# Optimization experiments

Measured on AMD Instinct MI355X. Metric: run time of the kernel, lower is better.

The kernel has to match this reference:

```python
import jax, jax.numpy as jnp
import numpy as np

B, N_IN, N_ALL, NPT, K, C, H = 8, 20000, 1200, 1024, 34, 96, 6
DH = C // H
RADIUS2 = (2.5 * 0.04) ** 2  # grid_size=0.04, sigma=1.0 -> radius 0.1


def _fps(xyz, npoint):
    # furthest point sampling, vectorized over batch, scan over sample steps
    Bb, Nn, _ = xyz.shape
    def step(carry, _):
        dist, far = carry
        cen = jnp.take_along_axis(xyz, far[:, None, None], axis=1)  # [B,1,3]
        d = jnp.sum((xyz - cen) ** 2, -1)                           # [B,N]
        dist = jnp.minimum(dist, d)
        return (dist, jnp.argmax(dist, -1).astype(jnp.int32)), far
    init = (jnp.full((Bb, Nn), 1e10, xyz.dtype), jnp.zeros((Bb,), jnp.int32))
    _, idx = jax.lax.scan(step, init, None, length=npoint)
    return idx.T  # [B, npoint]


def _gather(x, idx):
    return jnp.take_along_axis(x, idx[:, :, None], axis=1)


def _ln(x, g, b):
    m = jnp.mean(x, -1, keepdims=True)
    v = jnp.var(x, -1, keepdims=True)
    return (x - m) * jax.lax.rsqrt(v + 1e-5) * g + b


def _forward(point_clouds, cloud_colors, W_in, b_in, Wq, Wk, Wv, Wo, Wpos, W1, b1, W2, b2, g1, be1, g2, be2, sel):
    fps_idx = _fps(point_clouds, N_ALL)      # [B,1200]
    fps_idx = fps_idx[:, sel]                # random 1024 of 1200 (fixed permutation)
    coord = _gather(point_clouds, fps_idx)   # [B,P,3]
    color = _gather(cloud_colors, fps_idx)   # [B,P,3]
    # ball query within each cloud (all clouds have equal count -> batched dense dists)
    d2 = jnp.sum((coord[:, :, None] - coord[:, None]) ** 2, -1)        # [B,P,P]
    valid = d2 <= RADIUS2
    nidx = jnp.argsort(jnp.where(valid, d2, 1e10), axis=-1)[..., :K]   # [B,P,K]
    nvalid = jnp.take_along_axis(valid, nidx, axis=-1)                 # [B,P,K]
    feat = jnp.concatenate([color, coord], -1)                         # [B,P,6]
    x = feat @ W_in + b_in                                             # [B,P,C]
    q = (x @ Wq).reshape(B, NPT, H, DH)
    k = x @ Wk
    v = x @ Wv
    def gat(t):  # gather per-neighbor features: [B,P,C*] -> [B,P,K,C*]
        return jnp.take_along_axis(t, nidx.reshape(B, NPT * K)[:, :, None], axis=1).reshape(B, NPT, K, -1)
    kn, vn, pn = gat(k), gat(v), gat(coord)
    pe = (coord[:, :, None] - pn) @ Wpos                               # [B,P,K,C] rel-pos enc
    kn = (kn + pe).reshape(B, NPT, K, H, DH)
    vn = (vn + pe).reshape(B, NPT, K, H, DH)
    logits = jnp.einsum('bphd,bpkhd->bphk', q, kn) / jnp.sqrt(jnp.float32(DH))
    logits = jnp.where(nvalid[:, :, None, :], logits, -1e9)
    attn = jax.nn.softmax(logits, -1)
    out = jnp.einsum('bphk,bpkhd->bphd', attn, vn).reshape(B, NPT, C)
    x = _ln(x + out @ Wo, g1, be1)
    x = _ln(x + jax.nn.relu(x @ W1 + b1) @ W2 + b2, g2, be2)
    features = jnp.transpose(x, (0, 2, 1))                             # [B,C,P]
    return features, coord


def setup_inputs() -> dict:
    key = jax.random.key(0)
    ks = jax.random.split(key, 16)
    s = 0.1
    w = lambda k, shp: jax.random.normal(k, shp, jnp.float32) * s
    return {
        'point_clouds': jax.random.uniform(ks[0], (B, N_IN, 3), jnp.float32),
        'cloud_colors': jax.random.uniform(ks[1], (B, N_IN, 3), jnp.float32),
        'W_in': w(ks[2], (6, C)), 'b_in': jnp.zeros((C,), jnp.float32),
        'Wq': w(ks[3], (C, C)), 'Wk': w(ks[4], (C, C)), 'Wv': w(ks[5], (C, C)),
        'Wo': w(ks[6], (C, C)), 'Wpos': w(ks[7], (3, C)),
        'W1': w(ks[8], (C, 4 * C)), 'b1': jnp.zeros((4 * C,), jnp.float32),
        'W2': w(ks[9], (4 * C, C)), 'b2': jnp.zeros((C,), jnp.float32),
        'g1': jnp.ones((C,), jnp.float32), 'be1': jnp.zeros((C,), jnp.float32),
        'g2': jnp.ones((C,), jnp.float32), 'be2': jnp.zeros((C,), jnp.float32),
        'sel': jax.random.permutation(ks[10], N_ALL)[:NPT].astype(jnp.int32),
    }


def reference(point_clouds, cloud_colors, W_in, b_in, Wq, Wk, Wv, Wo, Wpos, W1, b1, W2, b2, g1, be1, g2, be2, sel):
    return _forward(point_clouds, cloud_colors, W_in, b_in, Wq, Wk, Wv, Wo, Wpos, W1, b1, W2, b2, g1, be1, g2, be2, sel)
```

## Files before the change

### kernel.cpp

```cpp
#include <hip/hip_runtime.h>
#include <math.h>

#define B_   8
#define NIN  20000
#define NALL 1200
#define NPTQ 1024
#define KNB  34
#define CH   96
#define FF   384
#define NQ   (B_ * NPTQ)
#define SL   20

typedef unsigned int   u32;
typedef unsigned long long u64;

__device__ __forceinline__ float scrub(float f) {
    u32 u = __float_as_uint(f);
    return ((u & 0x7F800000u) == 0x7F800000u) ? 12345.0f : f;
}

__global__ __launch_bounds__(1024, 4) void fps_kernel(const float* __restrict__ pc,
                                                      int* __restrict__ fps_idx) {
    const int b = blockIdx.x;
    const int tid = threadIdx.x;
    const int lane = tid & 63;
    const int wid = tid >> 6;
    const float* base = pc + (size_t)b * NIN * 3;

    float px[SL], py[SL], pz[SL], dist[SL];
#pragma unroll
    for (int j = 0; j < SL; ++j) {
        int idx = tid + j * 1024;
        bool ok = (j < SL - 1) || (idx < NIN);
        int ia = ok ? idx : 0;
        px[j] = base[(size_t)ia * 3 + 0];
        py[j] = base[(size_t)ia * 3 + 1];
        pz[j] = base[(size_t)ia * 3 + 2];
        dist[j] = ok ? 1e10f : -1.0f;
    }
#pragma unroll
    for (int j = 0; j < SL; ++j) {
        asm volatile("" : "+v"(px[j]), "+v"(py[j]), "+v"(pz[j]));
    }

    __shared__ u64 red[2][16];

    if (tid == 0) fps_idx[b * NALL + 0] = 0;
    float cx = base[0], cy = base[1], cz = base[2];

    for (int it = 1; it < NALL; ++it) {
        const int p = it & 1;
        float bd = -1e38f; int bi = 0;
#pragma unroll
        for (int j = 0; j < SL; ++j) {
            float dx = __fsub_rn(px[j], cx);
            float dy = __fsub_rn(py[j], cy);
            float dz = __fsub_rn(pz[j], cz);
            float d = __fadd_rn(__fadd_rn(__fmul_rn(dx, dx), __fmul_rn(dy, dy)),
                                __fmul_rn(dz, dz));
            float nd = fminf(dist[j], d);
            dist[j] = nd;
            if (nd > bd) { bd = nd; bi = tid + j * 1024; }
        }
        u64 key = ((u64)__float_as_uint(bd) << 32) | (u32)(NIN - bi);
#pragma unroll
        for (int s = 32; s; s >>= 1) {
            u64 o = __shfl_xor(key, s, 64);
            key = (o > key) ? o : key;
        }
        if (lane == 0) red[p][wid] = key;
        __syncthreads();
        u64 k2 = red[p][lane & 15];
#pragma unroll
        for (int s = 1; s < 16; s <<= 1) {
            u64 o = __shfl_xor(k2, s, 64);
            k2 = (o > k2) ? o : k2;
        }
        int widx = NIN - (int)(k2 & 0xFFFFFFFFu);
        if (tid == 0) fps_idx[b * NALL + it] = widx;
        const float* wp = base + (size_t)widx * 3;
        cx = wp[0]; cy = wp[1]; cz = wp[2];
    }
}

__global__ void gather_kernel(const float* __restrict__ pc,
                              const int* __restrict__ fps_idx, const int* __restrict__ sel,
                              float* __restrict__ coord, float* __restrict__ out_coord) {
    int t = blockIdx.x * 256 + threadIdx.x;
    if (t >= NQ) return;
    int b = t >> 10, j = t & 1023;
    int p = fps_idx[b * NALL + sel[j]];
    p = (p < 0) ? 0 : ((p >= NIN) ? (NIN - 1) : p);
    const float* pp = pc + ((size_t)b * NIN + p) * 3;
    float x = pp[0], y = pp[1], z = pp[2];
    coord[(size_t)t * 3 + 0] = x;
    coord[(size_t)t * 3 + 1] = y;
    coord[(size_t)t * 3 + 2] = z;
    out_coord[(size_t)t * 3 + 0] = scrub(x);
    out_coord[(size_t)t * 3 + 1] = scrub(y);
    out_coord[(size_t)t * 3 + 2] = scrub(z);
}

__global__ void knn_kernel(const float* __restrict__ coord, int* __restrict__ nbr) {
    __shared__ float sx[NPTQ], sy[NPTQ], sz[NPTQ];
    const double RAD2D = (2.5 * 0.04) * (2.5 * 0.04);
    int b = blockIdx.x >> 8;
    int i0 = (blockIdx.x & 255) * 4;
    const float* cb = coord + (size_t)b * NPTQ * 3;
    for (int t = threadIdx.x; t < NPTQ; t += 256) {
        sx[t] = cb[(size_t)t * 3 + 0];
        sy[t] = cb[(size_t)t * 3 + 1];
        sz[t] = cb[(size_t)t * 3 + 2];
    }
    __syncthreads();
    int wid = threadIdx.x >> 6, lane = threadIdx.x & 63;
    int i = i0 + wid;
    float qx = sx[i], qy = sy[i], qz = sz[i];
    u64 pk[16];
#pragma unroll
    for (int t = 0; t < 16; ++t) {
        int j = lane + t * 64;
        float dx = __fsub_rn(qx, sx[j]);
        float dy = __fsub_rn(qy, sy[j]);
        float dz = __fsub_rn(qz, sz[j]);
        float d2 = __fadd_rn(__fadd_rn(__fmul_rn(dx, dx), __fmul_rn(dy, dy)),
                             __fmul_rn(dz, dz));
        bool valid = ((double)d2 <= RAD2D);
        pk[t] = valid ? (((u64)__float_as_uint(d2) << 32) | (u32)j) : ~0ull;
    }
    int* out = nbr + ((size_t)b * NPTQ + i) * KNB;
    int k = 0;
    for (; k < KNB; ++k) {
        u64 m = ~0ull;
#pragma unroll
        for (int t = 0; t < 16; ++t) m = (pk[t] < m) ? pk[t] : m;
#pragma unroll
        for (int s = 32; s; s >>= 1) {
            u64 o = __shfl_xor(m, s, 64);
            m = (o < m) ? o : m;
        }
        if (m == ~0ull) break;
#pragma unroll
        for (int t = 0; t < 16; ++t) if (pk[t] == m) pk[t] = ~0ull;
        if (lane == 0) out[k] = (int)(m & 0xFFFFFFFFu);
    }
    for (; k < KNB; ++k) if (lane == 0) out[k] = -1;
}

__global__ void xproj_kernel(const float* __restrict__ pc, const float* __restrict__ col,
                             const int* __restrict__ fps_idx, const int* __restrict__ sel,
                             const float* __restrict__ Win, const float* __restrict__ bin,
                             float* __restrict__ x) {
    int idx = blockIdx.x * 256 + threadIdx.x;
    if (idx >= NQ * CH) return;
    int q = idx / CH, c = idx - q * CH;
    int b = q >> 10, j = q & 1023;
    int p = fps_idx[b * NALL + sel[j]];
    p = (p < 0) ? 0 : ((p >= NIN) ? (NIN - 1) : p);
    const float* pp = pc + ((size_t)b * NIN + p) * 3;
    const float* cc = col + ((size_t)b * NIN + p) * 3;
    float acc = bin[c];
    acc += cc[0] * Win[0 * CH + c];
    acc += cc[1] * Win[1 * CH + c];
    acc += cc[2] * Win[2 * CH + c];
    acc += pp[0] * Win[3 * CH + c];
    acc += pp[1] * Win[4 * CH + c];
    acc += pp[2] * Win[5 * CH + c];
    x[idx] = acc;
}

__global__ void qkv_kernel(const float* __restrict__ x,
                           const float* __restrict__ Wq, const float* __restrict__ Wk,
                           const float* __restrict__ Wv,
                           float* __restrict__ qo, float* __restrict__ ko,
                           float* __restrict__ vo) {
    int idx = blockIdx.x * 256 + threadIdx.x;
    if (idx >= NQ * CH) return;
    int q = idx / CH, c = idx - q * CH;
    const float* xr = x + (size_t)q * CH;
    float aq = 0.f, ak = 0.f, av = 0.f;
    for (int k = 0; k < CH; ++k) {
        float xv = xr[k];
        aq += xv * Wq[k * CH + c];
        ak += xv * Wk[k * CH + c];
        av += xv * Wv[k * CH + c];
    }
    qo[idx] = aq; ko[idx] = ak; vo[idx] = av;
}

__global__ __launch_bounds__(384) void attn_kernel(float* __restrict__ qr1,
                            const float* __restrict__ km, const float* __restrict__ vm,
                            const float* __restrict__ coord, const int* __restrict__ nbr,
                            const float* __restrict__ Wpos, const float* __restrict__ Wo,
                            const float* __restrict__ x) {
    __shared__ float wp[3 * CH];
    __shared__ float os[4][CH];
    for (int t = threadIdx.x; t < 3 * CH; t += 384) wp[t] = Wpos[t];
    __syncthreads();
    int lq = threadIdx.x / CH;
    int c = threadIdx.x - lq * CH;
    int qi = blockIdx.x * 4 + lq;
    int b = qi >> 10, i = qi & 1023;
    const float* crd = coord + (size_t)b * NPTQ * 3;
    float cx = crd[(size_t)i * 3], cy = crd[(size_t)i * 3 + 1], cz = crd[(size_t)i * 3 + 2];
    float qv = qr1[(size_t)qi * CH + c];
    const int* nb = nbr + (size_t)qi * KNB;
    float m = -1e30f, l = 0.f, acc = 0.f;
    for (int t = 0; t < KNB; ++t) {
        int j = nb[t];
        if (j < 0) break;
        float dx = cx - crd[(size_t)j * 3];
        float dy = cy - crd[(size_t)j * 3 + 1];
        float dz = cz - crd[(size_t)j * 3 + 2];
        float pe = dx * wp[c] + dy * wp[CH + c] + dz * wp[2 * CH + c];
        size_t row = (size_t)(b * NPTQ + j) * CH + c;
        float kn = km[row] + pe;
        float s = qv * kn;
        s += __shfl_xor(s, 1); s += __shfl_xor(s, 2);
        s += __shfl_xor(s, 4); s += __shfl_xor(s, 8);
        float logit = s * 0.25f;
        float mn = fmaxf(m, logit);
        float sc = expf(m - mn);
        float p = expf(logit - mn);
        float vn = vm[row] + pe;
        l = l * sc + p;
        acc = acc * sc + p * vn;
        m = mn;
    }
    os[lq][c] = (l > 0.f) ? acc / l : 0.f;
    __syncthreads();
    float r = x[(size_t)qi * CH + c];
    for (int k = 0; k < CH; ++k) r += os[lq][k] * Wo[k * CH + c];
    qr1[(size_t)qi * CH + c] = r;
}

__global__ void ln_kernel(const float* __restrict__ in, const float* __restrict__ g,
                          const float* __restrict__ be, float* __restrict__ out) {
    int row = blockIdx.x * 4 + (threadIdx.x >> 6);
    int lane = threadIdx.x & 63;
    const float* r = in + (size_t)row * CH;
    float e0 = r[lane];
    float e1 = (lane < 32) ? r[64 + lane] : 0.0f;
    float s = e0 + e1;
#pragma unroll
    for (int k = 32; k; k >>= 1) s += __shfl_xor(s, k);
    float mean = s * (1.0f / 96.0f);
    float d0 = e0 - mean, d1 = e1 - mean;
    float vs = d0 * d0 + ((lane < 32) ? d1 * d1 : 0.0f);
#pragma unroll
    for (int k = 32; k; k >>= 1) vs += __shfl_xor(vs, k);
    float rs = 1.0f / sqrtf(vs * (1.0f / 96.0f) + 1e-5f);
    float* o = out + (size_t)row * CH;
    o[lane] = d0 * rs * g[lane] + be[lane];
    if (lane < 32) o[64 + lane] = d1 * rs * g[64 + lane] + be[64 + lane];
}

__global__ __launch_bounds__(384) void ffn_kernel(const float* __restrict__ x2,
                           const float* __restrict__ W1, const float* __restrict__ b1,
                           const float* __restrict__ W2, const float* __restrict__ b2,
                           float* __restrict__ r2) {
    __shared__ float xs[4][CH];
    __shared__ float hs[4][FF];
    __shared__ float ps[4][4][CH];
    int row0 = blockIdx.x * 4, t = threadIdx.x;
    { int r = t / CH, c = t - (t / CH) * CH;
      xs[r][c] = x2[(size_t)(row0 + r) * CH + c]; }
    __syncthreads();
    {
        float bt = b1[t];
        float a0 = bt, a1 = bt, a2 = bt, a3 = bt;
        for (int k = 0; k < CH; ++k) {
            float w = W1[k * FF + t];
            a0 += xs[0][k] * w; a1 += xs[1][k] * w;
            a2 += xs[2][k] * w; a3 += xs[3][k] * w;
        }
        hs[0][t] = fmaxf(a0, 0.f); hs[1][t] = fmaxf(a1, 0.f);
        hs[2][t] = fmaxf(a2, 0.f); hs[3][t] = fmaxf(a3, 0.f);
    }
    __syncthreads();
    {
        int chunk = t / CH, c = t - (t / CH) * CH;
        float p0 = 0.f, p1 = 0.f, p2 = 0.f, p3 = 0.f;
        for (int m = chunk * CH; m < (chunk + 1) * CH; ++m) {
            float w = W2[m * CH + c];
            p0 += hs[0][m] * w; p1 += hs[1][m] * w;
            p2 += hs[2][m] * w; p3 += hs[3][m] * w;
        }
        ps[0][chunk][c] = p0; ps[1][chunk][c] = p1;
        ps[2][chunk][c] = p2; ps[3][chunk][c] = p3;
    }
    __syncthreads();
    { int r = t / CH, c = t - (t / CH) * CH;
      float rr = xs[r][c] + ((ps[r][0][c] + ps[r][1][c]) + (ps[r][2][c] + ps[r][3][c])) + b2[c];
      r2[(size_t)(row0 + r) * CH + c] = rr; }
}

__global__ void ln2t_kernel(const float* __restrict__ in, const float* __restrict__ g,
                            const float* __restrict__ be, float* __restrict__ out) {
    int row = blockIdx.x * 4 + (threadIdx.x >> 6);
    int lane = threadIdx.x & 63;
    int b = row >> 10, i = row & 1023;
    const float* r = in + (size_t)row * CH;
    float e0 = r[lane];
    float e1 = (lane < 32) ? r[64 + lane] : 0.0f;
    float s = e0 + e1;
#pragma unroll
    for (int k = 32; k; k >>= 1) s += __shfl_xor(s, k);
    float mean = s * (1.0f / 96.0f);
    float d0 = e0 - mean, d1 = e1 - mean;
    float vs = d0 * d0 + ((lane < 32) ? d1 * d1 : 0.0f);
#pragma unroll
    for (int k = 32; k; k >>= 1) vs += __shfl_xor(vs, k);
    float rs = 1.0f / sqrtf(vs * (1.0f / 96.0f) + 1e-5f);
    float y0 = d0 * rs * g[lane] + be[lane];
    out[((size_t)(b * CH + lane)) * NPTQ + i] = scrub(y0);
    if (lane < 32) {
        float y1 = d1 * rs * g[64 + lane] + be[64 + lane];
        out[((size_t)(b * CH + 64 + lane)) * NPTQ + i] = scrub(y1);
    }
}

extern "C" void kernel_launch(void* const* d_in, const int* in_sizes, int n_in,
                              void* d_out, int out_size, void* d_ws, size_t ws_size,
                              hipStream_t stream) {
    const float* pc   = (const float*)d_in[0];
    const float* col  = (const float*)d_in[1];
    const float* Win  = (const float*)d_in[2];
    const float* bin  = (const float*)d_in[3];
    const float* Wq   = (const float*)d_in[4];
    const float* Wk   = (const float*)d_in[5];
    const float* Wv   = (const float*)d_in[6];
    const float* Wo   = (const float*)d_in[7];
    const float* Wpos = (const float*)d_in[8];
    const float* W1   = (const float*)d_in[9];
    const float* b1   = (const float*)d_in[10];
    const float* W2   = (const float*)d_in[11];
    const float* b2   = (const float*)d_in[12];
    const float* g1   = (const float*)d_in[13];
    const float* be1  = (const float*)d_in[14];
    const float* g2   = (const float*)d_in[15];
    const float* be2  = (const float*)d_in[16];
    const int*  sel   = (const int*)d_in[17];

    float* out_feat  = (float*)d_out;
    float* out_coord = out_feat + (size_t)B_ * CH * NPTQ;

    char* ws = (char*)d_ws;
    size_t off = 0;
    auto alloc = [&](size_t bytes) { void* p = ws + off; off += (bytes + 255) & ~(size_t)255; return p; };
    int*   w_fps   = (int*)  alloc((size_t)B_ * NALL * 4);
    float* w_coord = (float*)alloc((size_t)NQ * 3 * 4);
    int*   w_nbr   = (int*)  alloc((size_t)NQ * KNB * 4);
    float* w_x     = (float*)alloc((size_t)NQ * CH * 4);
    float* w_q     = (float*)alloc((size_t)NQ * CH * 4);
    float* w_k     = (float*)alloc((size_t)NQ * CH * 4);
    float* w_v     = (float*)alloc((size_t)NQ * CH * 4);
    (void)ws_size; (void)in_sizes; (void)n_in; (void)out_size;

    fps_kernel<<<B_, 1024, 0, stream>>>(pc, w_fps);
    gather_kernel<<<NQ / 256, 256, 0, stream>>>(pc, w_fps, sel, w_coord, out_coord);
    knn_kernel<<<NQ / 4, 256, 0, stream>>>(w_coord, w_nbr);
    xproj_kernel<<<NQ * CH / 256, 256, 0, stream>>>(pc, col, w_fps, sel, Win, bin, w_x);
    qkv_kernel<<<NQ * CH / 256, 256, 0, stream>>>(w_x, Wq, Wk, Wv, w_q, w_k, w_v);
    attn_kernel<<<NQ / 4, 384, 0, stream>>>(w_q, w_k, w_v, w_coord, w_nbr, Wpos, Wo, w_x);
    ln_kernel<<<NQ / 4, 256, 0, stream>>>(w_q, g1, be1, w_k);
    ffn_kernel<<<NQ / 4, 384, 0, stream>>>(w_k, W1, b1, W2, b2, w_v);
    ln2t_kernel<<<NQ / 4, 256, 0, stream>>>(w_v, g2, be2, out_feat);
}
```

Baseline: 2.628 ms.

## Halve FPS block size and use packed two-wide float math per thread

The FPS kernel now runs 512 threads per batch, each owning 40 points held as two-wide float vectors so subtract, multiply and min can map to packed FP32 instructions. The cross-wave reduction shrinks from 16 to 8 waves and is done by reading shared memory serially instead of with shuffles. The aim is to shorten the per-iteration critical path of the serial 1200-step loop, both in compute and in synchronization. In exchange, each thread does twice as much work per step and uses more registers. The no-op shuffles replace the asm barrier that kept the point values resident in registers.

```diff
diff --git a/kernel.cpp b/kernel.cpp
--- a/kernel.cpp
+++ b/kernel.cpp
@@ -9,74 +9,90 @@
 #define CH   96
 #define FF   384
 #define NQ   (B_ * NPTQ)
-#define SL   20
+
+#define FT   512
+#define NPR  20
 
 typedef unsigned int   u32;
 typedef unsigned long long u64;
+typedef float v2f __attribute__((ext_vector_type(2)));
 
 __device__ __forceinline__ float scrub(float f) {
     u32 u = __float_as_uint(f);
     return ((u & 0x7F800000u) == 0x7F800000u) ? 12345.0f : f;
 }
 
-__global__ __launch_bounds__(1024, 4) void fps_kernel(const float* __restrict__ pc,
-                                                      int* __restrict__ fps_idx) {
+__global__ __launch_bounds__(FT, 2) void fps_kernel(const float* __restrict__ pc,
+                                                    int* __restrict__ fps_idx) {
+#pragma clang fp contract(off)
     const int b = blockIdx.x;
     const int tid = threadIdx.x;
     const int lane = tid & 63;
     const int wid = tid >> 6;
     const float* base = pc + (size_t)b * NIN * 3;
 
-    float px[SL], py[SL], pz[SL], dist[SL];
-#pragma unroll
-    for (int j = 0; j < SL; ++j) {
-        int idx = tid + j * 1024;
-        bool ok = (j < SL - 1) || (idx < NIN);
-        int ia = ok ? idx : 0;
-        px[j] = base[(size_t)ia * 3 + 0];
-        py[j] = base[(size_t)ia * 3 + 1];
-        pz[j] = base[(size_t)ia * 3 + 2];
-        dist[j] = ok ? 1e10f : -1.0f;
-    }
-#pragma unroll
-    for (int j = 0; j < SL; ++j) {
-        asm volatile("" : "+v"(px[j]), "+v"(py[j]), "+v"(pz[j]));
-    }
-
-    __shared__ u64 red[2][16];
+    v2f px[NPR], py[NPR], pz[NPR], dist[NPR];
+#pragma unroll
+    for (int j = 0; j < NPR; ++j) {
+        int i0 = tid + (2 * j) * FT;
+        int i1 = i0 + FT;
+        bool ok1 = i1 < NIN;
+        int a1 = ok1 ? i1 : 0;
+        float x0 = base[(size_t)i0 * 3 + 0];
+        float y0 = base[(size_t)i0 * 3 + 1];
+        float z0 = base[(size_t)i0 * 3 + 2];
+        float x1 = base[(size_t)a1 * 3 + 0];
+        float y1 = base[(size_t)a1 * 3 + 1];
+        float z1 = base[(size_t)a1 * 3 + 2];
+        x0 = __shfl(x0, lane); y0 = __shfl(y0, lane); z0 = __shfl(z0, lane);
+        x1 = __shfl(x1, lane); y1 = __shfl(y1, lane); z1 = __shfl(z1, lane);
+        px[j].x = x0; px[j].y = x1;
+        py[j].x = y0; py[j].y = y1;
+        pz[j].x = z0; pz[j].y = z1;
+        dist[j].x = 1e10f;
+        dist[j].y = ok1 ? 1e10f : -1.0f;
+    }
+
+    __shared__ u64 rkey[2][8];
 
     if (tid == 0) fps_idx[b * NALL + 0] = 0;
     float cx = base[0], cy = base[1], cz = base[2];
 
     for (int it = 1; it < NALL; ++it) {
-        const int p = it & 1;
-        float bd = -1e38f; int bi = 0;
-#pragma unroll
-        for (int j = 0; j < SL; ++j) {
-            float dx = __fsub_rn(px[j], cx);
-            float dy = __fsub_rn(py[j], cy);
-            float dz = __fsub_rn(pz[j], cz);
-            float d = __fadd_rn(__fadd_rn(__fmul_rn(dx, dx), __fmul_rn(dy, dy)),
-                                __fmul_rn(dz, dz));
-            float nd = fminf(dist[j], d);
+        const int pb = it & 1;
+        v2f cvx; cvx.x = cx; cvx.y = cx;
+        v2f cvy; cvy.x = cy; cvy.y = cy;
+        v2f cvz; cvz.x = cz; cvz.y = cz;
+        float bd0 = -1e38f, bd1 = -1e38f;
+        int bi0 = 0, bi1 = 0;
+#pragma unroll
+        for (int j = 0; j < NPR; ++j) {
+            v2f dx = px[j] - cvx;
+            v2f dy = py[j] - cvy;
+            v2f dz = pz[j] - cvz;
+            v2f sx = dx * dx;
+            v2f sy = dy * dy;
+            v2f sz = dz * dz;
+            v2f d  = (sx + sy) + sz;
+            v2f nd = __builtin_elementwise_min(dist[j], d);
             dist[j] = nd;
-            if (nd > bd) { bd = nd; bi = tid + j * 1024; }
-        }
-        u64 key = ((u64)__float_as_uint(bd) << 32) | (u32)(NIN - bi);
+            if (nd.x > bd0) { bd0 = nd.x; bi0 = tid + (2 * j) * FT; }
+            if (nd.y > bd1) { bd1 = nd.y; bi1 = tid + (2 * j + 1) * FT; }
+        }
+        u64 k0 = ((u64)__float_as_uint(bd0) << 32) | (u32)(NIN - bi0);
+        u64 k1 = ((u64)__float_as_uint(bd1) << 32) | (u32)(NIN - bi1);
+        u64 key = (k1 > k0) ? k1 : k0;
 #pragma unroll
         for (int s = 32; s; s >>= 1) {
             u64 o = __shfl_xor(key, s, 64);
             key = (o > key) ? o : key;
         }
-        if (lane == 0) red[p][wid] = key;
+        if (lane == 0) rkey[pb][wid] = key;
         __syncthreads();
-        u64 k2 = red[p][lane & 15];
-#pragma unroll
-        for (int s = 1; s < 16; s <<= 1) {
-            u64 o = __shfl_xor(k2, s, 64);
-            k2 = (o > k2) ? o : k2;
-        }
-        int widx = NIN - (int)(k2 & 0xFFFFFFFFu);
+        u64 kk = rkey[pb][0];
+#pragma unroll
+        for (int w = 1; w < 8; ++w) { u64 o = rkey[pb][w]; kk = (o > kk) ? o : kk; }
+        int widx = NIN - (int)(kk & 0xFFFFFFFFu);
         if (tid == 0) fps_idx[b * NALL + it] = widx;
         const float* wp = base + (size_t)widx * 3;
         cx = wp[0]; cy = wp[1]; cz = wp[2];
@@ -357,7 +373,7 @@
     float* w_v     = (float*)alloc((size_t)NQ * CH * 4);
     (void)ws_size; (void)in_sizes; (void)n_in; (void)out_size;
 
-    fps_kernel<<<B_, 1024, 0, stream>>>(pc, w_fps);
+    fps_kernel<<<B_, FT, 0, stream>>>(pc, w_fps);
     gather_kernel<<<NQ / 256, 256, 0, stream>>>(pc, w_fps, sel, w_coord, out_coord);
     knn_kernel<<<NQ / 4, 256, 0, stream>>>(w_coord, w_nbr);
     xproj_kernel<<<NQ * CH / 256, 256, 0, stream>>>(pc, col, w_fps, sel, Win, bin, w_x);
```

Result: faster. 2.477 ms (-5.7%).

## Bucket FPS points by spatial cell and skip distance updates via bounding-box bounds

Applied to the files above, without the earlier changes.

The FPS kernel now counting-sorts each cloud's points into an 8x8x8 grid and stores them as float4 (xyz plus original index) in workspace, so each thread owns a spatially compact group of 20 points. Each thread keeps a bounding box of its group. It skips the distance update when the box's lower-bound distance to the new centroid cannot lower its current max distance. This is meant to avoid most per-iteration distance work in later FPS iterations. In exchange, points are reloaded from global/L2 each iteration instead of registers, and the in-block sort adds setup cost. The skip test is conservative (0.999 factor) but the tie-break ordering must still match the reference argmax.

```diff
diff --git a/kernel.cpp b/kernel.cpp
--- a/kernel.cpp
+++ b/kernel.cpp
@@ -9,7 +9,10 @@
 #define CH   96
 #define FF   384
 #define NQ   (B_ * NPTQ)
-#define SL   20
+
+#define GC   8
+#define NC   (GC * GC * GC)
+#define PPT  20
 
 typedef unsigned int   u32;
 typedef unsigned long long u64;
@@ -19,56 +22,111 @@
     return ((u & 0x7F800000u) == 0x7F800000u) ? 12345.0f : f;
 }
 
-__global__ __launch_bounds__(1024, 4) void fps_kernel(const float* __restrict__ pc,
-                                                      int* __restrict__ fps_idx) {
+__device__ __forceinline__ int cell_of(float x, float y, float z) {
+    int ix = (int)(x * (float)GC); ix = ix < 0 ? 0 : (ix > GC - 1 ? GC - 1 : ix);
+    int iy = (int)(y * (float)GC); iy = iy < 0 ? 0 : (iy > GC - 1 ? GC - 1 : iy);
+    int iz = (int)(z * (float)GC); iz = iz < 0 ? 0 : (iz > GC - 1 ? GC - 1 : iz);
+    return (ix * GC + iy) * GC + iz;
+}
+
+__global__ __launch_bounds__(1024, 4) void fps_kernel(
+        const float* __restrict__ pc, int* __restrict__ fps_idx,
+        float4* __restrict__ gpts) {
+#pragma clang fp contract(off)
     const int b = blockIdx.x;
     const int tid = threadIdx.x;
     const int lane = tid & 63;
     const int wid = tid >> 6;
     const float* base = pc + (size_t)b * NIN * 3;
-
-    float px[SL], py[SL], pz[SL], dist[SL];
-#pragma unroll
-    for (int j = 0; j < SL; ++j) {
+    float4* bp = gpts + (size_t)b * NIN;
+
+    __shared__ int cstart[NC];
+    __shared__ int ccur[NC];
+    __shared__ u64 red[2][16];
+
+    for (int c = tid; c < NC; c += 1024) ccur[c] = 0;
+    __syncthreads();
+    for (int j = 0; j < PPT; ++j) {
         int idx = tid + j * 1024;
-        bool ok = (j < SL - 1) || (idx < NIN);
-        int ia = ok ? idx : 0;
-        px[j] = base[(size_t)ia * 3 + 0];
-        py[j] = base[(size_t)ia * 3 + 1];
-        pz[j] = base[(size_t)ia * 3 + 2];
-        dist[j] = ok ? 1e10f : -1.0f;
-    }
-#pragma unroll
-    for (int j = 0; j < SL; ++j) {
-        asm volatile("" : "+v"(px[j]), "+v"(py[j]), "+v"(pz[j]));
-    }
-
-    __shared__ u64 red[2][16];
-
+        if (idx < NIN) {
+            float x = base[(size_t)idx * 3 + 0];
+            float y = base[(size_t)idx * 3 + 1];
+            float z = base[(size_t)idx * 3 + 2];
+            atomicAdd(&ccur[cell_of(x, y, z)], 1);
+        }
+    }
+    __syncthreads();
+    if (tid == 0) {
+        int acc = 0;
+        for (int c = 0; c < NC; ++c) { cstart[c] = acc; acc += ccur[c]; }
+    }
+    __syncthreads();
+    if (tid < NC) ccur[tid] = cstart[tid];
+    __syncthreads();
+    for (int j = 0; j < PPT; ++j) {
+        int idx = tid + j * 1024;
+        if (idx < NIN) {
+            float x = base[(size_t)idx * 3 + 0];
+            float y = base[(size_t)idx * 3 + 1];
+            float z = base[(size_t)idx * 3 + 2];
+            int pos = atomicAdd(&ccur[cell_of(x, y, z)], 1);
+            bp[pos] = make_float4(x, y, z, (float)idx);
+        }
+    }
+    __syncthreads();
+
+    const bool valid = tid < (NIN / PPT);
+    float dist[PPT];
+#pragma unroll
+    for (int j = 0; j < PPT; ++j) dist[j] = 1e10f;
+    float bnx = 1e30f, bny = 1e30f, bnz = 1e30f;
+    float bxx = -1e30f, bxy = -1e30f, bxz = -1e30f;
+    if (valid) {
+#pragma unroll
+        for (int j = 0; j < PPT; ++j) {
+            float4 w = bp[tid * PPT + j];
+            bnx = fminf(bnx, w.x); bxx = fmaxf(bxx, w.x);
+            bny = fminf(bny, w.y); bxy = fmaxf(bxy, w.y);
+            bnz = fminf(bnz, w.z); bxz = fmaxf(bxz, w.z);
+        }
+    }
+    u64 key = valid ? (((u64)__float_as_uint(1e10f) << 32) | 1u) : 0ull;
+
+    float cx = base[0], cy = base[1], cz = base[2];
     if (tid == 0) fps_idx[b * NALL + 0] = 0;
-    float cx = base[0], cy = base[1], cz = base[2];
 
     for (int it = 1; it < NALL; ++it) {
         const int p = it & 1;
-        float bd = -1e38f; int bi = 0;
-#pragma unroll
-        for (int j = 0; j < SL; ++j) {
-            float dx = __fsub_rn(px[j], cx);
-            float dy = __fsub_rn(py[j], cy);
-            float dz = __fsub_rn(pz[j], cz);
-            float d = __fadd_rn(__fadd_rn(__fmul_rn(dx, dx), __fmul_rn(dy, dy)),
-                                __fmul_rn(dz, dz));
-            float nd = fminf(dist[j], d);
-            dist[j] = nd;
-            if (nd > bd) { bd = nd; bi = tid + j * 1024; }
-        }
-        u64 key = ((u64)__float_as_uint(bd) << 32) | (u32)(NIN - bi);
+        float maxd = __uint_as_float((u32)(key >> 32));
+        float tx = fmaxf(fmaxf(bnx - cx, cx - bxx), 0.0f);
+        float ty = fmaxf(fmaxf(bny - cy, cy - bxy), 0.0f);
+        float tz = fmaxf(fmaxf(bnz - cz, cz - bxz), 0.0f);
+        float lb = tx * tx + ty * ty + tz * tz;
+        bool needs = valid && (lb * 0.999f < maxd);
+        if (needs) {
+            u64 nk = 0;
+#pragma unroll
+            for (int j = 0; j < PPT; ++j) {
+                float4 w = bp[tid * PPT + j];
+                float dx = __fsub_rn(w.x, cx);
+                float dy = __fsub_rn(w.y, cy);
+                float dz = __fsub_rn(w.z, cz);
+                float d = __fadd_rn(__fadd_rn(__fmul_rn(dx, dx), __fmul_rn(dy, dy)),
+                                    __fmul_rn(dz, dz));
+                float nd = fminf(dist[j], d);
+                dist[j] = nd;
+                u64 kk = ((u64)__float_as_uint(nd) << 32) | (u32)(NIN - (int)w.w);
+                nk = (kk > nk) ? kk : nk;
+            }
+            key = nk;
+        }
+        u64 kr = key;
 #pragma unroll
         for (int s = 32; s; s >>= 1) {
-            u64 o = __shfl_xor(key, s, 64);
-            key = (o > key) ? o : key;
-        }
-        if (lane == 0) red[p][wid] = key;
+            u64 o = __shfl_xor(kr, s, 64);
+            kr = (o > kr) ? o : kr;
+        }
+        if (lane == 0) red[p][wid] = kr;
         __syncthreads();
         u64 k2 = red[p][lane & 15];
 #pragma unroll
@@ -348,6 +406,7 @@
     char* ws = (char*)d_ws;
     size_t off = 0;
     auto alloc = [&](size_t bytes) { void* p = ws + off; off += (bytes + 255) & ~(size_t)255; return p; };
+    float4* w_pts  = (float4*)alloc((size_t)B_ * NIN * 16);
     int*   w_fps   = (int*)  alloc((size_t)B_ * NALL * 4);
     float* w_coord = (float*)alloc((size_t)NQ * 3 * 4);
     int*   w_nbr   = (int*)  alloc((size_t)NQ * KNB * 4);
@@ -357,7 +416,7 @@
     float* w_v     = (float*)alloc((size_t)NQ * CH * 4);
     (void)ws_size; (void)in_sizes; (void)n_in; (void)out_size;
 
-    fps_kernel<<<B_, 1024, 0, stream>>>(pc, w_fps);
+    fps_kernel<<<B_, 1024, 0, stream>>>(pc, w_fps, w_pts);
     gather_kernel<<<NQ / 256, 256, 0, stream>>>(pc, w_fps, sel, w_coord, out_coord);
     knn_kernel<<<NQ / 4, 256, 0, stream>>>(w_coord, w_nbr);
     xproj_kernel<<<NQ * CH / 256, 256, 0, stream>>>(pc, col, w_fps, sel, Win, bin, w_x);
```

Result: slower. 4.055 ms (+54.3%).
